# Optimization experiments

Hardware: AMD Instinct MI355X
Metric: run time of the kernel (lower is better)

## Reference

```python
import jax, jax.numpy as jnp
import numpy as np
from jax.scipy.special import erfc

LMBDA = 0.01
K = 3
_NEG_INV_SQRT2 = -0.7071067811865476  # -2**(-0.5)


def _std_cdf(t):
    # Numerically stable Gaussian CDF via erfc, matching torch impl.
    return 0.5 * erfc(_NEG_INV_SQRT2 * t)


def setup_inputs() -> dict:
    key = jax.random.key(0)
    k1, k2, k3, k4, k5 = jax.random.split(key, 5)
    B, C, H, W = 16, 192, 48, 48
    img = 768
    return {
        "x": jax.random.uniform(k1, (B, 3, img, img), dtype=jnp.float32),
        "x_hat": jax.random.uniform(k2, (B, 3, img, img), dtype=jnp.float32),
        "params": jax.random.normal(k3, (B, C * 3 * K, H, W), dtype=jnp.float32),
        "y_hat": jax.random.normal(k4, (B, C, H, W), dtype=jnp.float32),
        "z_hat": jax.random.normal(k5, (B, C, 12, 12), dtype=jnp.float32),
    }


def _latent_rate_gmm(y, params):
    B, C, H, W = y.shape
    p = params.reshape(B, C, 3, K, H, W)
    log_weights = jax.nn.log_softmax(p[:, :, 0], axis=2)      # [B,C,K,H,W]
    means = p[:, :, 1]
    scales = jnp.clip(jnp.exp(p[:, :, 2]), 1e-5)
    y_exp = y[:, :, None]                                      # [B,C,1,H,W]
    upper = (y_exp + 0.5 - means) / scales
    lower = (y_exp - 0.5 - means) / scales
    pmf_k = jnp.clip(_std_cdf(upper) - _std_cdf(lower), 1e-6)
    log_pmf_total = jax.nn.logsumexp(log_weights + jnp.log(pmf_k), axis=2)
    return -log_pmf_total / jnp.log(jnp.float32(2.0))          # bits, [B,C,H,W]


def _hyperlatent_rate(z):
    pmf = jnp.clip(_std_cdf(z + 0.5) - _std_cdf(z - 0.5), 1e-6)
    return -jnp.log2(pmf)


def reference(x, x_hat, params, y_hat, z_hat):
    distortion = jnp.mean((x_hat - x) ** 2)
    rate_y = _latent_rate_gmm(y_hat, params).sum(axis=(1, 2, 3)).mean()
    rate_z = _hyperlatent_rate(z_hat).sum(axis=(1, 2, 3)).mean()
    num_pixels = x.shape[0] * x.shape[2] * x.shape[3]
    bpp_loss = (rate_y + rate_z) / num_pixels
    loss = LMBDA * (255.0 ** 2) * distortion + bpp_loss
    return (loss, distortion, bpp_loss)
```

## Files before the change

kernel.cpp:

```cpp
#include <hip/hip_runtime.h>
#include <math.h>

#define BB 16
#define CC 192
#define KK 3
#define HH 48
#define WW 48
#define HW (HH * WW)
#define N_Y (BB * CC * HW)
#define IMG 768
#define N_X (BB * 3 * IMG * IMG)
#define N_Z (BB * CC * 12 * 12)
#define NUM_PIXELS (BB * IMG * IMG)

#define INV_SQRT2 0.7071067811865476f

#define G_GMM   (N_Y / (256 * 8))
#define G_MSE   1728
#define G_HYP   (N_Z / (256 * 8))
#define G_TOTAL (G_GMM + G_MSE + G_HYP)
#define SWIZZLE_PRIME 7919

typedef float v4f __attribute__((ext_vector_type(4)));

__device__ __forceinline__ float erf_fast(float x) {
    float ax = fabsf(x);
    float t  = __builtin_amdgcn_rcpf(fmaf(0.3275911f, ax, 1.0f));
    float p  = t * fmaf(t, fmaf(t, fmaf(t, fmaf(t, 1.061405429f,
                 -1.453152027f), 1.421413741f), -0.284496736f), 0.254829592f);
    float e  = __expf(-ax * ax);
    float r  = fmaf(-p, e, 1.0f);
    return copysignf(r, x);
}

__device__ __forceinline__ void block_write_partial(double* __restrict__ slot,
                                                    float val) {
    #pragma unroll
    for (int off = 32; off > 0; off >>= 1)
        val += __shfl_down(val, off, 64);
    __shared__ float smem[4];
    int lane = threadIdx.x & 63;
    int wid  = threadIdx.x >> 6;
    if (lane == 0) smem[wid] = val;
    __syncthreads();
    if (threadIdx.x == 0) {
        float s = smem[0] + smem[1] + smem[2] + smem[3];
        *slot = (double)s;
    }
}

__device__ __forceinline__ float gmm_rate(float y,
                                          float w0, float w1, float w2,
                                          float m0, float m1, float m2,
                                          float s0, float s1, float s2) {
    float mw = fmaxf(w0, fmaxf(w1, w2));
    float e0 = __expf(w0 - mw), e1 = __expf(w1 - mw), e2 = __expf(w2 - mw);
    float S = e0 + e1 + e2;

    float i0 = fminf(__expf(-s0), 1e5f) * INV_SQRT2;
    float i1 = fminf(__expf(-s1), 1e5f) * INV_SQRT2;
    float i2 = fminf(__expf(-s2), 1e5f) * INV_SQRT2;

    float yu = y + 0.5f, yl = y - 0.5f;

    float d0 = erf_fast((yu - m0) * i0) - erf_fast((yl - m0) * i0);
    float d1 = erf_fast((yu - m1) * i1) - erf_fast((yl - m1) * i1);
    float d2 = erf_fast((yu - m2) * i2) - erf_fast((yl - m2) * i2);

    float P = e0 * fmaxf(d0, 2e-6f);
    P = fmaf(e1, fmaxf(d1, 2e-6f), P);
    P = fmaf(e2, fmaxf(d2, 2e-6f), P);

    return __log2f(S) - __log2f(P) + 1.0f;
}

__global__ void __launch_bounds__(256)
fused_kernel(const float* __restrict__ x, const float* __restrict__ xh,
             const float* __restrict__ params, const float* __restrict__ y_hat,
             const float* __restrict__ z_hat, double* __restrict__ partial) {
    unsigned v = ((unsigned)blockIdx.x * SWIZZLE_PRIME) % G_TOTAL;

    if (v < G_GMM) {
        v4f y4[2];
        v4f f[2][9];
        #pragma unroll
        for (int h = 0; h < 2; ++h) {
            int gid = v * 512 + h * 256 + threadIdx.x;
            int bc  = gid / (HW / 4);
            int hw4 = gid - bc * (HW / 4);
            const v4f* pp = (const v4f*)params + (size_t)bc * (9 * HW / 4) + hw4;
            y4[h] = ((const v4f*)y_hat)[gid];
            #pragma unroll
            for (int s = 0; s < 9; ++s)
                f[h][s] = pp[s * (HW / 4)];
        }
        float r = 0.0f;
        #pragma unroll
        for (int h = 0; h < 2; ++h)
            #pragma unroll
            for (int c = 0; c < 4; ++c)
                r += gmm_rate(y4[h][c], f[h][0][c], f[h][1][c], f[h][2][c],
                              f[h][3][c], f[h][4][c], f[h][5][c],
                              f[h][6][c], f[h][7][c], f[h][8][c]);
        block_write_partial(&partial[v], r);
    } else if (v < G_GMM + G_MSE) {
        int mb = v - G_GMM;
        const v4f* x4  = (const v4f*)x;
        const v4f* xh4 = (const v4f*)xh;
        size_t base = (size_t)mb * 4096 + threadIdx.x;
        float a0 = 0.f, a1 = 0.f, a2 = 0.f, a3 = 0.f;
        #pragma unroll
        for (int it = 0; it < 4; ++it) {
            size_t b0 = base + (size_t)it * 1024;
            v4f p0 = __builtin_nontemporal_load(x4  + b0);
            v4f p1 = __builtin_nontemporal_load(x4  + b0 + 256);
            v4f p2 = __builtin_nontemporal_load(x4  + b0 + 512);
            v4f p3 = __builtin_nontemporal_load(x4  + b0 + 768);
            v4f q0 = __builtin_nontemporal_load(xh4 + b0);
            v4f q1 = __builtin_nontemporal_load(xh4 + b0 + 256);
            v4f q2 = __builtin_nontemporal_load(xh4 + b0 + 512);
            v4f q3 = __builtin_nontemporal_load(xh4 + b0 + 768);
            v4f d0 = q0 - p0, d1 = q1 - p1, d2 = q2 - p2, d3 = q3 - p3;
            a0 += d0.x*d0.x + d0.y*d0.y + d0.z*d0.z + d0.w*d0.w;
            a1 += d1.x*d1.x + d1.y*d1.y + d1.z*d1.z + d1.w*d1.w;
            a2 += d2.x*d2.x + d2.y*d2.y + d2.z*d2.z + d2.w*d2.w;
            a3 += d3.x*d3.x + d3.y*d3.y + d3.z*d3.z + d3.w*d3.w;
        }
        block_write_partial(&partial[v], (a0 + a1) + (a2 + a3));
    } else {
        int hb = v - G_GMM - G_MSE;
        int g  = hb * 512 + threadIdx.x;
        v4f z0 = ((const v4f*)z_hat)[g];
        v4f z1 = ((const v4f*)z_hat)[g + 256];
        float r = 0.0f;
        #pragma unroll
        for (int j = 0; j < 8; ++j) {
            float z = (j < 4) ? z0[j] : z1[j - 4];
            float d = erf_fast((z + 0.5f) * INV_SQRT2)
                    - erf_fast((z - 0.5f) * INV_SQRT2);
            r += 1.0f - __log2f(fmaxf(d, 2e-6f));
        }
        block_write_partial(&partial[v], r);
    }
}

__global__ void __launch_bounds__(256)
finalize_kernel(const double* __restrict__ partial, float* __restrict__ out) {
    __shared__ double sm[256];
    double seg[3];
    const int lo[3] = {0, G_GMM, G_GMM + G_MSE};
    const int hi[3] = {G_GMM, G_GMM + G_MSE, G_TOTAL};
    for (int k = 0; k < 3; ++k) {
        double a = 0.0;
        for (int i = lo[k] + threadIdx.x; i < hi[k]; i += 256) a += partial[i];
        sm[threadIdx.x] = a;
        __syncthreads();
        for (int off = 128; off > 0; off >>= 1) {
            if (threadIdx.x < (unsigned)off) sm[threadIdx.x] += sm[threadIdx.x + off];
            __syncthreads();
        }
        seg[k] = sm[0];
        __syncthreads();
    }
    if (threadIdx.x == 0) {
        double rate_y     = seg[0];
        double sq_err     = seg[1];
        double rate_z     = seg[2];
        double distortion = sq_err / (double)N_X;
        double bpp = (rate_y / (double)BB + rate_z / (double)BB) / (double)NUM_PIXELS;
        double loss = 0.01 * 255.0 * 255.0 * distortion + bpp;
        out[0] = (float)loss;
        out[1] = (float)distortion;
        out[2] = (float)bpp;
    }
}

extern "C" void kernel_launch(void* const* d_in, const int* in_sizes, int n_in,
                              void* d_out, int out_size, void* d_ws, size_t ws_size,
                              hipStream_t stream) {
    const float* x      = (const float*)d_in[0];
    const float* x_hat  = (const float*)d_in[1];
    const float* params = (const float*)d_in[2];
    const float* y_hat  = (const float*)d_in[3];
    const float* z_hat  = (const float*)d_in[4];
    float* out = (float*)d_out;
    double* partial = (double*)d_ws;

    fused_kernel<<<G_TOTAL, 256, 0, stream>>>(x, x_hat, params, y_hat, z_hat, partial);
    finalize_kernel<<<1, 256, 0, stream>>>(partial, out);
}
```

Measured before the change: 499.1 us.

## Convert fused loss kernel to persistent grid-stride with software-pipelined loads

Replaces the swizzled one-block-per-tile dispatch with a fixed 1024-block persistent grid. Each thread processes GMM, MSE and hyperlatent work in sequence, double-buffering GMM loads and prefetching MSE loads two iterations ahead, with sched barriers to enforce the ordering. Per-block partials for all three terms are reduced together at the end. The aim is to overlap memory latency with the erf/exp compute and to cut block-launch and reduction overhead. The trade-off is a limited prefetch depth in the MSE stream and higher register pressure.

```diff
diff --git a/kernel.cpp b/kernel.cpp
--- a/kernel.cpp
+++ b/kernel.cpp
@@ -3,7 +3,6 @@
 
 #define BB 16
 #define CC 192
-#define KK 3
 #define HH 48
 #define WW 48
 #define HW (HH * WW)
@@ -15,13 +14,20 @@
 
 #define INV_SQRT2 0.7071067811865476f
 
-#define G_GMM   (N_Y / (256 * 8))
-#define G_MSE   1728
-#define G_HYP   (N_Z / (256 * 8))
-#define G_TOTAL (G_GMM + G_MSE + G_HYP)
-#define SWIZZLE_PRIME 7919
+#define GRID 1024
+#define TPB  256
+#define NTH  (GRID * TPB)
+
+#define GMM_U    (N_Y / 4)
+#define GMM_FULL 6
+#define GMM_TAIL (GMM_U - GMM_FULL * NTH)
+#define MSE_U    (N_X / 4)
+#define MSE_IT   (MSE_U / NTH)
+#define HYP_U    (N_Z / 4)
 
 typedef float v4f __attribute__((ext_vector_type(4)));
+
+#define SBAR() __builtin_amdgcn_sched_barrier(0)
 
 __device__ __forceinline__ float erf_fast(float x) {
     float ax = fabsf(x);
@@ -33,22 +39,6 @@
     return copysignf(r, x);
 }
 
-__device__ __forceinline__ void block_write_partial(double* __restrict__ slot,
-                                                    float val) {
-    #pragma unroll
-    for (int off = 32; off > 0; off >>= 1)
-        val += __shfl_down(val, off, 64);
-    __shared__ float smem[4];
-    int lane = threadIdx.x & 63;
-    int wid  = threadIdx.x >> 6;
-    if (lane == 0) smem[wid] = val;
-    __syncthreads();
-    if (threadIdx.x == 0) {
-        float s = smem[0] + smem[1] + smem[2] + smem[3];
-        *slot = (double)s;
-    }
-}
-
 __device__ __forceinline__ float gmm_rate(float y,
                                           float w0, float w1, float w2,
                                           float m0, float m1, float m2,
@@ -74,73 +64,102 @@
     return __log2f(S) - __log2f(P) + 1.0f;
 }
 
-__global__ void __launch_bounds__(256)
+#define GMM_LOAD(S, U) do {                                              \
+    int bc_ = (U) / 576;                                                 \
+    int hw_ = (U) - bc_ * 576;                                           \
+    const v4f* pp_ = params4 + (size_t)bc_ * 5184 + hw_;                 \
+    S##y = y4p[(U)];                                                     \
+    S##0 = pp_[0 * 576]; S##1 = pp_[1 * 576]; S##2 = pp_[2 * 576];       \
+    S##3 = pp_[3 * 576]; S##4 = pp_[4 * 576]; S##5 = pp_[5 * 576];       \
+    S##6 = pp_[6 * 576]; S##7 = pp_[7 * 576]; S##8 = pp_[8 * 576];       \
+} while (0)
+
+#define GMM_COMP(S, ACC) do {                                            \
+    float r_ = 0.0f;                                                     \
+    _Pragma("unroll")                                                    \
+    for (int c_ = 0; c_ < 4; ++c_)                                       \
+        r_ += gmm_rate(S##y[c_], S##0[c_], S##1[c_], S##2[c_],           \
+                       S##3[c_], S##4[c_], S##5[c_],                     \
+                       S##6[c_], S##7[c_], S##8[c_]);                    \
+    ACC += r_;                                                           \
+} while (0)
+
+__global__ void __launch_bounds__(TPB, 4)
 fused_kernel(const float* __restrict__ x, const float* __restrict__ xh,
              const float* __restrict__ params, const float* __restrict__ y_hat,
              const float* __restrict__ z_hat, double* __restrict__ partial) {
-    unsigned v = ((unsigned)blockIdx.x * SWIZZLE_PRIME) % G_TOTAL;
-
-    if (v < G_GMM) {
-        v4f y4[2];
-        v4f f[2][9];
-        #pragma unroll
-        for (int h = 0; h < 2; ++h) {
-            int gid = v * 512 + h * 256 + threadIdx.x;
-            int bc  = gid / (HW / 4);
-            int hw4 = gid - bc * (HW / 4);
-            const v4f* pp = (const v4f*)params + (size_t)bc * (9 * HW / 4) + hw4;
-            y4[h] = ((const v4f*)y_hat)[gid];
-            #pragma unroll
-            for (int s = 0; s < 9; ++s)
-                f[h][s] = pp[s * (HW / 4)];
-        }
-        float r = 0.0f;
-        #pragma unroll
-        for (int h = 0; h < 2; ++h)
-            #pragma unroll
-            for (int c = 0; c < 4; ++c)
-                r += gmm_rate(y4[h][c], f[h][0][c], f[h][1][c], f[h][2][c],
-                              f[h][3][c], f[h][4][c], f[h][5][c],
-                              f[h][6][c], f[h][7][c], f[h][8][c]);
-        block_write_partial(&partial[v], r);
-    } else if (v < G_GMM + G_MSE) {
-        int mb = v - G_GMM;
+    const int tid = blockIdx.x * TPB + threadIdx.x;
+    const v4f* params4 = (const v4f*)params;
+    const v4f* y4p     = (const v4f*)y_hat;
+
+    float accG = 0.0f, accM = 0.0f, accH = 0.0f;
+
+    {
+        v4f Ay, A0, A1, A2, A3, A4, A5, A6, A7, A8;
+        v4f By, B0, B1, B2, B3, B4, B5, B6, B7, B8;
+        int u = tid;
+        GMM_LOAD(A, u);
+        GMM_LOAD(B, u + 1 * NTH); SBAR(); GMM_COMP(A, accG);
+        GMM_LOAD(A, u + 2 * NTH); SBAR(); GMM_COMP(B, accG);
+        GMM_LOAD(B, u + 3 * NTH); SBAR(); GMM_COMP(A, accG);
+        GMM_LOAD(A, u + 4 * NTH); SBAR(); GMM_COMP(B, accG);
+        GMM_LOAD(B, u + 5 * NTH); SBAR(); GMM_COMP(A, accG);
+        if (tid < GMM_TAIL) { GMM_LOAD(A, u + 6 * NTH); }
+        SBAR(); GMM_COMP(B, accG);
+        if (tid < GMM_TAIL) { SBAR(); GMM_COMP(A, accG); }
+    }
+
+    {
         const v4f* x4  = (const v4f*)x;
         const v4f* xh4 = (const v4f*)xh;
-        size_t base = (size_t)mb * 4096 + threadIdx.x;
-        float a0 = 0.f, a1 = 0.f, a2 = 0.f, a3 = 0.f;
+        v4f pA = __builtin_nontemporal_load(x4  + tid);
+        v4f qA = __builtin_nontemporal_load(xh4 + tid);
+        v4f pB = __builtin_nontemporal_load(x4  + tid + NTH);
+        v4f qB = __builtin_nontemporal_load(xh4 + tid + NTH);
+        v4f pC, qC;
         #pragma unroll
-        for (int it = 0; it < 4; ++it) {
-            size_t b0 = base + (size_t)it * 1024;
-            v4f p0 = __builtin_nontemporal_load(x4  + b0);
-            v4f p1 = __builtin_nontemporal_load(x4  + b0 + 256);
-            v4f p2 = __builtin_nontemporal_load(x4  + b0 + 512);
-            v4f p3 = __builtin_nontemporal_load(x4  + b0 + 768);
-            v4f q0 = __builtin_nontemporal_load(xh4 + b0);
-            v4f q1 = __builtin_nontemporal_load(xh4 + b0 + 256);
-            v4f q2 = __builtin_nontemporal_load(xh4 + b0 + 512);
-            v4f q3 = __builtin_nontemporal_load(xh4 + b0 + 768);
-            v4f d0 = q0 - p0, d1 = q1 - p1, d2 = q2 - p2, d3 = q3 - p3;
-            a0 += d0.x*d0.x + d0.y*d0.y + d0.z*d0.z + d0.w*d0.w;
-            a1 += d1.x*d1.x + d1.y*d1.y + d1.z*d1.z + d1.w*d1.w;
-            a2 += d2.x*d2.x + d2.y*d2.y + d2.z*d2.z + d2.w*d2.w;
-            a3 += d3.x*d3.x + d3.y*d3.y + d3.z*d3.z + d3.w*d3.w;
+        for (int it = 0; it < MSE_IT; ++it) {
+            if (it + 2 < MSE_IT) {
+                int gn = tid + (it + 2) * NTH;
+                pC = __builtin_nontemporal_load(x4  + gn);
+                qC = __builtin_nontemporal_load(xh4 + gn);
+            }
+            SBAR();
+            v4f d = qA - pA;
+            accM += d.x * d.x + d.y * d.y + d.z * d.z + d.w * d.w;
+            pA = pB; qA = qB; pB = pC; qB = qC;
         }
-        block_write_partial(&partial[v], (a0 + a1) + (a2 + a3));
-    } else {
-        int hb = v - G_GMM - G_MSE;
-        int g  = hb * 512 + threadIdx.x;
-        v4f z0 = ((const v4f*)z_hat)[g];
-        v4f z1 = ((const v4f*)z_hat)[g + 256];
-        float r = 0.0f;
+    }
+
+    if (tid < HYP_U) {
+        v4f z4 = ((const v4f*)z_hat)[tid];
         #pragma unroll
-        for (int j = 0; j < 8; ++j) {
-            float z = (j < 4) ? z0[j] : z1[j - 4];
+        for (int j = 0; j < 4; ++j) {
+            float z = z4[j];
             float d = erf_fast((z + 0.5f) * INV_SQRT2)
                     - erf_fast((z - 0.5f) * INV_SQRT2);
-            r += 1.0f - __log2f(fmaxf(d, 2e-6f));
+            accH += 1.0f - __log2f(fmaxf(d, 2e-6f));
         }
-        block_write_partial(&partial[v], r);
+    }
+
+    #pragma unroll
+    for (int off = 32; off > 0; off >>= 1) {
+        accG += __shfl_down(accG, off, 64);
+        accM += __shfl_down(accM, off, 64);
+        accH += __shfl_down(accH, off, 64);
+    }
+    __shared__ float sm[4][3];
+    int lane = threadIdx.x & 63;
+    int wid  = threadIdx.x >> 6;
+    if (lane == 0) { sm[wid][0] = accG; sm[wid][1] = accM; sm[wid][2] = accH; }
+    __syncthreads();
+    if (threadIdx.x == 0) {
+        partial[blockIdx.x] =
+            (double)(sm[0][0] + sm[1][0] + sm[2][0] + sm[3][0]);
+        partial[GRID + blockIdx.x] =
+            (double)(sm[0][1] + sm[1][1] + sm[2][1] + sm[3][1]);
+        partial[2 * GRID + blockIdx.x] =
+            (double)(sm[0][2] + sm[1][2] + sm[2][2] + sm[3][2]);
     }
 }
 
@@ -148,8 +167,8 @@
 finalize_kernel(const double* __restrict__ partial, float* __restrict__ out) {
     __shared__ double sm[256];
     double seg[3];
-    const int lo[3] = {0, G_GMM, G_GMM + G_MSE};
-    const int hi[3] = {G_GMM, G_GMM + G_MSE, G_TOTAL};
+    const int lo[3] = {0, GRID, 2 * GRID};
+    const int hi[3] = {GRID, 2 * GRID, 3 * GRID};
     for (int k = 0; k < 3; ++k) {
         double a = 0.0;
         for (int i = lo[k] + threadIdx.x; i < hi[k]; i += 256) a += partial[i];
@@ -186,6 +205,6 @@
     float* out = (float*)d_out;
     double* partial = (double*)d_ws;
 
-    fused_kernel<<<G_TOTAL, 256, 0, stream>>>(x, x_hat, params, y_hat, z_hat, partial);
+    fused_kernel<<<GRID, TPB, 0, stream>>>(x, x_hat, params, y_hat, z_hat, partial);
     finalize_kernel<<<1, 256, 0, stream>>>(partial, out);
 }
```

New measurement: 578.1 us. +15.8%, slower.
